# Optimization experiments

Measured on AMD Instinct MI355X. Metric: run time of the kernel, lower is better.

## Reference

```python
import jax, jax.numpy as jnp
import numpy as np

D_MODEL = 1024
N_HEADS = 16
HEAD_DIM = D_MODEL // N_HEADS
THETA = 10000.0


def _rope_tables(seq_len, d_k, dtype):
    pos = jnp.arange(seq_len, dtype=jnp.float32)
    dim = jnp.arange(0, d_k, 2, dtype=jnp.float32)
    inv_freq = 1.0 / (THETA ** (dim / d_k))  # [d_k//2]
    angle = pos[:, None] * inv_freq[None, :]  # [seq, d_k//2]
    return jnp.cos(angle).astype(dtype), jnp.sin(angle).astype(dtype)


def _apply_rope(x, cos, sin):
    # x: [B, H, S, d_k]; cos/sin: [S, d_k//2] (interleaved-pair rotation)
    x1 = x[..., ::2]
    x2 = x[..., 1::2]
    r1 = x1 * cos - x2 * sin
    r2 = x1 * sin + x2 * cos
    out = jnp.stack([r1, r2], axis=-1)  # [..., d_k//2, 2]
    return out.reshape(x.shape)


def setup_inputs() -> dict:
    key = jax.random.key(0)
    ks = jax.random.split(key, 5)
    B, S, D = 4, 2048, D_MODEL
    std = np.sqrt(2.0 / (D + D)).astype(np.float32)
    x = jax.random.normal(ks[0], (B, S, D), dtype=jnp.float32)
    wq = jax.random.normal(ks[1], (D, D), dtype=jnp.float32) * std
    wk = jax.random.normal(ks[2], (D, D), dtype=jnp.float32) * std
    wv = jax.random.normal(ks[3], (D, D), dtype=jnp.float32) * std
    wo = jax.random.normal(ks[4], (D, D), dtype=jnp.float32) * std
    return {"x": x, "wq": wq, "wk": wk, "wv": wv, "wo": wo}


def reference(x, wq, wk, wv, wo):
    B, S, D = x.shape
    H, dk = N_HEADS, HEAD_DIM
    # projections (weight stored [d_out, d_in])
    q = jnp.einsum('oi,bsi->bso', wq, x)
    k = jnp.einsum('oi,bsi->bso', wk, x)
    v = jnp.einsum('oi,bsi->bso', wv, x)
    # split heads -> [B, H, S, dk]
    q = q.reshape(B, S, H, dk).transpose(0, 2, 1, 3)
    k = k.reshape(B, S, H, dk).transpose(0, 2, 1, 3)
    v = v.reshape(B, S, H, dk).transpose(0, 2, 1, 3)
    cos, sin = _rope_tables(S, dk, x.dtype)
    q = _apply_rope(q, cos, sin)
    k = _apply_rope(k, cos, sin)
    scale = 1.0 / np.sqrt(dk)
    logits = jnp.einsum('bhqd,bhkd->bhqk', q, k) * scale
    causal = jnp.tril(jnp.ones((S, S), dtype=bool))
    logits = jnp.where(causal, logits, -jnp.inf)
    probs = jax.nn.softmax(logits, axis=-1)
    ctx = jnp.einsum('bhqk,bhkd->bhqd', probs, v)
    ctx = ctx.transpose(0, 2, 1, 3).reshape(B, S, D)
    return jnp.einsum('oi,bsi->bso', wo, ctx)
```

## Files before the change

### kernel.cpp

```cpp
#include <hip/hip_runtime.h>
#include <hip/hip_bf16.h>
#include <cstdint>
#include <cstddef>


typedef __bf16 bf16;
typedef __bf16 bf16x2 __attribute__((ext_vector_type(2)));
typedef __bf16 bf16x4 __attribute__((ext_vector_type(4)));
typedef __bf16 bf16x8 __attribute__((ext_vector_type(8)));
typedef float  f32x4  __attribute__((ext_vector_type(4)));

#define SEQ 2048
#define NH  16
#define DM  1024
#define MFMA16 __builtin_amdgcn_mfma_f32_16x16x32_bf16

__device__ __forceinline__ void async16(bf16* lds, const bf16* g) {
  __builtin_amdgcn_global_load_lds(
      (__attribute__((address_space(1))) void*)(g),
      (__attribute__((address_space(3))) void*)(lds), 16, 0, 0);
}

__global__ void cvt_all(const float* __restrict__ x,
                        const float* __restrict__ w0, const float* __restrict__ w1,
                        const float* __restrict__ w2, const float* __restrict__ w3,
                        bf16* __restrict__ xb, bf16* __restrict__ wb) {
  int i = blockIdx.x * blockDim.x + threadIdx.x;
  float4 f;
  bf16x4* dst;
  if (i < 2097152) {
    f = ((const float4*)x)[i];
    dst = (bf16x4*)xb + i;
  } else {
    int k = i - 2097152;
    int sel = k >> 18, j = k & 262143;
    const float* src = sel == 0 ? w0 : sel == 1 ? w1 : sel == 2 ? w2 : w3;
    f = ((const float4*)src)[j];
    dst = (bf16x4*)wb + k;
  }
  bf16x4 o;
  o.x = (bf16)f.x; o.y = (bf16)f.y; o.z = (bf16)f.z; o.w = (bf16)f.w;
  *dst = o;
}


__global__ void __launch_bounds__(256)
gemm_out(const bf16* __restrict__ A, const bf16* __restrict__ B,
         float* __restrict__ C, int M, int N, int K) {
  __shared__ bf16 As[3][128 * 32];
  __shared__ bf16 Bs[3][128 * 32];
  const int tid  = threadIdx.x;
  const int lane = tid & 63;
  const int w    = tid >> 6;
  const int l15  = lane & 15, g = lane >> 4;
  const int wr   = w >> 1, wc = w & 1;
  const long bm = (long)blockIdx.x * 128, bn = (long)blockIdx.y * 128;

  f32x4 acc[4][4] = {};

  const int r0 = tid >> 2;
  const int c0 = (tid & 3) << 3;
  const bf16* aB = A + (bm + r0) * K + c0;
  const bf16* bB = B + (bn + r0) * K + c0;

#pragma unroll
  for (int t = 0; t < 2; ++t) {
    const bf16* ap = aB + t * 32;
    const bf16* bp = bB + t * 32;
    async16(&As[t][(size_t)tid * 8],        ap);
    async16(&As[t][2048 + (size_t)tid * 8], ap + (size_t)64 * K);
    async16(&Bs[t][(size_t)tid * 8],        bp);
    async16(&Bs[t][2048 + (size_t)tid * 8], bp + (size_t)64 * K);
  }

  const int nkt = K >> 5;
  int cur = 0;
  for (int kt = 0; kt < nkt; ++kt) {
    if (kt + 1 < nkt) asm volatile("s_waitcnt vmcnt(4)" ::: "memory");
    else              asm volatile("s_waitcnt vmcnt(0)" ::: "memory");
    __builtin_amdgcn_s_barrier();
    asm volatile("" ::: "memory");
    if (kt + 2 < nkt) {
      const int nb = (cur == 0) ? 2 : cur - 1;
      const bf16* ap = aB + (kt + 2) * 32;
      const bf16* bp = bB + (kt + 2) * 32;
      async16(&As[nb][(size_t)tid * 8],        ap);
      async16(&As[nb][2048 + (size_t)tid * 8], ap + (size_t)64 * K);
      async16(&Bs[nb][(size_t)tid * 8],        bp);
      async16(&Bs[nb][2048 + (size_t)tid * 8], bp + (size_t)64 * K);
    }
    bf16x8 af[4], bfr[4];
#pragma unroll
    for (int mf = 0; mf < 4; ++mf)
      af[mf] = *(const bf16x8*)&As[cur][(wr * 64 + mf * 16 + l15) * 32 + g * 8];
#pragma unroll
    for (int nf = 0; nf < 4; ++nf)
      bfr[nf] = *(const bf16x8*)&Bs[cur][(wc * 64 + nf * 16 + l15) * 32 + g * 8];
#pragma unroll
    for (int mf = 0; mf < 4; ++mf)
#pragma unroll
      for (int nf = 0; nf < 4; ++nf)
        acc[mf][nf] = MFMA16(af[mf], bfr[nf], acc[mf][nf], 0, 0, 0);
    cur = (cur == 2) ? 0 : cur + 1;
  }

#pragma unroll
  for (int mf = 0; mf < 4; ++mf)
#pragma unroll
    for (int nf = 0; nf < 4; ++nf)
#pragma unroll
      for (int r = 0; r < 4; ++r) {
        long m = bm + wr * 64 + mf * 16 + g * 4 + r;
        long n = bn + wc * 64 + nf * 16 + l15;
        C[m * N + n] = acc[mf][nf][r];
      }
}

__global__ void __launch_bounds__(256)
gemm_qkv(const bf16* __restrict__ A, const bf16* __restrict__ Wqkv,
         bf16* __restrict__ Qo, bf16* __restrict__ Ko, bf16* __restrict__ Vto,
         int M, int K) {
  __shared__ bf16 As[3][128 * 32];
  __shared__ bf16 Bs[3][128 * 32];
  const int tid  = threadIdx.x;
  const int lane = tid & 63;
  const int w    = tid >> 6;
  const int l15  = lane & 15, g = lane >> 4;
  const int wr   = w >> 1, wc = w & 1;
  const long bm  = (long)blockIdx.x * 128;
  const long bnG = (long)blockIdx.y * 128;
  const int region = blockIdx.y >> 3;
  const long bn  = (long)(blockIdx.y & 7) * 128;

  f32x4 acc[4][4] = {};

  const int r0 = tid >> 2;
  const int c0 = (tid & 3) << 3;
  const bf16* aB = A + (bm + r0) * K + c0;
  const bf16* bB = Wqkv + (bnG + r0) * K + c0;

#pragma unroll
  for (int t = 0; t < 2; ++t) {
    const bf16* ap = aB + t * 32;
    const bf16* bp = bB + t * 32;
    async16(&As[t][(size_t)tid * 8],        ap);
    async16(&As[t][2048 + (size_t)tid * 8], ap + (size_t)64 * K);
    async16(&Bs[t][(size_t)tid * 8],        bp);
    async16(&Bs[t][2048 + (size_t)tid * 8], bp + (size_t)64 * K);
  }

  const int nkt = K >> 5;
  int cur = 0;
  for (int kt = 0; kt < nkt; ++kt) {
    if (kt + 1 < nkt) asm volatile("s_waitcnt vmcnt(4)" ::: "memory");
    else              asm volatile("s_waitcnt vmcnt(0)" ::: "memory");
    __builtin_amdgcn_s_barrier();
    asm volatile("" ::: "memory");
    if (kt + 2 < nkt) {
      const int nb = (cur == 0) ? 2 : cur - 1;
      const bf16* ap = aB + (kt + 2) * 32;
      const bf16* bp = bB + (kt + 2) * 32;
      async16(&As[nb][(size_t)tid * 8],        ap);
      async16(&As[nb][2048 + (size_t)tid * 8], ap + (size_t)64 * K);
      async16(&Bs[nb][(size_t)tid * 8],        bp);
      async16(&Bs[nb][2048 + (size_t)tid * 8], bp + (size_t)64 * K);
    }
    bf16x8 af[4], bfr[4];
#pragma unroll
    for (int mf = 0; mf < 4; ++mf)
      af[mf] = *(const bf16x8*)&As[cur][(wr * 64 + mf * 16 + l15) * 32 + g * 8];
#pragma unroll
    for (int nf = 0; nf < 4; ++nf)
      bfr[nf] = *(const bf16x8*)&Bs[cur][(wc * 64 + nf * 16 + l15) * 32 + g * 8];
#pragma unroll
    for (int mf = 0; mf < 4; ++mf)
#pragma unroll
      for (int nf = 0; nf < 4; ++nf)
        acc[mf][nf] = MFMA16(af[mf], bfr[nf], acc[mf][nf], 0, 0, 0);
    cur = (cur == 2) ? 0 : cur + 1;
  }

  if (region < 2) {
    bf16* C = region ? Ko : Qo;
#pragma unroll
    for (int mf = 0; mf < 4; ++mf)
#pragma unroll
      for (int nf = 0; nf < 4; ++nf)
#pragma unroll
        for (int r = 0; r < 4; ++r) {
          long m = bm + wr * 64 + mf * 16 + g * 4 + r;
          long n = bn + wc * 64 + nf * 16 + l15;
          C[m * DM + n] = (bf16)acc[mf][nf][r];
        }
  } else {
#pragma unroll
    for (int mf = 0; mf < 4; ++mf)
#pragma unroll
      for (int nf = 0; nf < 4; ++nf) {
        long s0 = bm + wr * 64 + mf * 16 + g * 4;
        long b  = s0 >> 11;
        long s  = s0 & 2047;
        long n  = bn + wc * 64 + nf * 16 + l15;
        long h  = n >> 6, d = n & 63;
        bf16x4 v;
#pragma unroll
        for (int r = 0; r < 4; ++r) v[r] = (bf16)acc[mf][nf][r];
        *(bf16x4*)&Vto[(((b * NH + h) * 64 + d) << 11) + s] = v;
      }
  }
}

__global__ void rope_k(bf16* __restrict__ K) {
  int i = blockIdx.x * blockDim.x + threadIdx.x;
  size_t e = (size_t)i * 8;
  const int d0 = (int)(e & 63);
  const int s  = (int)((e >> 10) & 2047);
  bf16x8 v = *(bf16x8*)&K[e];
#pragma unroll
  for (int t = 0; t < 4; ++t) {
    const int j = (d0 >> 1) + t;
    float inv = __expf((float)j * -0.2878231366242558f);
    float ang = (float)s * inv;
    float sn, cn;
    __sincosf(ang, &sn, &cn);
    float k1 = (float)v[2 * t], k2 = (float)v[2 * t + 1];
    v[2 * t]     = (bf16)(k1 * cn - k2 * sn);
    v[2 * t + 1] = (bf16)(k1 * sn + k2 * cn);
  }
  *(bf16x8*)&K[e] = v;
}

__global__ void __launch_bounds__(256, 2)
attn_kernel(const bf16* __restrict__ Q, const bf16* __restrict__ Kg,
            const bf16* __restrict__ Vt, bf16* __restrict__ ctx) {
  __shared__ bf16 Ks[2][64 * 64];
  __shared__ bf16 Vs[2][64 * 64];
  __shared__ bf16 Ps[4 * 2048];
  const int tid  = threadIdx.x;
  const int lane = tid & 63, w = tid >> 6;
  const int l15  = lane & 15, g = lane >> 4;
  const int bid  = (int)blockIdx.x;
  const int qts  = 15 - (bid >> 6);
  const int bh   = bid & 63;
  const int b  = bh >> 4, h = bh & 15;
  const int qw = qts * 128 + w * 32;
  const int ktmax = 2 * qts + 1;

  bf16x8 qf[2][2];
#pragma unroll
  for (int qg = 0; qg < 2; ++qg) {
    const int srq = qw + qg * 16 + l15;
    const bf16* qp = Q + ((size_t)(b * SEQ + srq)) * DM + h * 64 + g * 8;
#pragma unroll
    for (int kk = 0; kk < 2; ++kk) {
      bf16x8 v = *(const bf16x8*)(qp + kk * 32);
#pragma unroll
      for (int t = 0; t < 4; ++t) {
        const int j = kk * 16 + g * 4 + t;
        float inv = __expf((float)j * -0.2878231366242558f);
        float ang = (float)srq * inv;
        float sn, cn;
        __sincosf(ang, &sn, &cn);
        float q1 = (float)v[2 * t], q2 = (float)v[2 * t + 1];
        v[2 * t]     = (bf16)((q1 * cn - q2 * sn) * 0.125f);
        v[2 * t + 1] = (bf16)((q1 * sn + q2 * cn) * 0.125f);
      }
      qf[qg][kk] = v;
    }
  }

  f32x4 o[2][4] = {};
  float l_run[2] = {0.f, 0.f};

  const int srow = tid >> 3, scc = tid & 7;
  const int swc  = 8 * (scc ^ (srow & 7));
  const bf16* kb0 = Kg + ((size_t)(b * SEQ + srow)) * DM + h * 64 + swc;
  const bf16* vb0 = Vt + ((size_t)(bh * 64 + srow)) * SEQ + swc;
  bf16* Pw = &Ps[w * 2048];

  async16(&Ks[0][(size_t)tid * 8],        kb0);
  async16(&Ks[0][2048 + (size_t)tid * 8], kb0 + (size_t)32 * DM);
  async16(&Vs[0][(size_t)tid * 8],        vb0);
  async16(&Vs[0][2048 + (size_t)tid * 8], vb0 + (size_t)32 * SEQ);

  for (int kt = 0; kt <= ktmax; ++kt) {
    const int kv0 = kt * 64;
    const int cur = kt & 1, nxt = cur ^ 1;
    __syncthreads();
    if (kt < ktmax) {
      const bf16* kp = kb0 + (size_t)(kt + 1) * 64 * DM;
      const bf16* vp = vb0 + (size_t)(kt + 1) * 64;
      async16(&Ks[nxt][(size_t)tid * 8],        kp);
      async16(&Ks[nxt][2048 + (size_t)tid * 8], kp + (size_t)32 * DM);
      async16(&Vs[nxt][(size_t)tid * 8],        vp);
      async16(&Vs[nxt][2048 + (size_t)tid * 8], vp + (size_t)32 * SEQ);
    }

    if (kv0 > qw + 31) continue;

    f32x4 sa[2][4] = {};
    __builtin_amdgcn_s_setprio(1);
#pragma unroll
    for (int kk = 0; kk < 2; ++kk)
#pragma unroll
      for (int mf = 0; mf < 4; ++mf) {
        const int row = mf * 16 + l15;
        bf16x8 kf = *(const bf16x8*)&Ks[cur][row * 64 + 8 * ((kk * 4 + g) ^ (row & 7))];
        sa[0][mf] = MFMA16(kf, qf[0][kk], sa[0][mf], 0, 0, 0);
        sa[1][mf] = MFMA16(kf, qf[1][kk], sa[1][mf], 0, 0, 0);
      }
    __builtin_amdgcn_s_setprio(0);

#pragma unroll
    for (int j = 0; j < 2; ++j) {
      const int qg = j;
      float p[16];
#pragma unroll
      for (int mf = 0; mf < 4; ++mf)
#pragma unroll
        for (int r = 0; r < 4; ++r) p[mf * 4 + r] = sa[j][mf][r];
      if (kv0 + 63 > qw + qg * 16) {
        const int qidx = qw + qg * 16 + l15;
#pragma unroll
        for (int mf = 0; mf < 4; ++mf)
#pragma unroll
          for (int r = 0; r < 4; ++r)
            if (kv0 + mf * 16 + g * 4 + r > qidx) p[mf * 4 + r] = -1e30f;
      }
      float ts = 0.f;
#pragma unroll
      for (int i = 0; i < 16; ++i) { p[i] = __expf(p[i] - 8.0f); ts += p[i]; }
      l_run[qg] += ts;
#pragma unroll
      for (int mf = 0; mf < 4; ++mf) {
        bf16x4 pv;
#pragma unroll
        for (int r = 0; r < 4; ++r) pv[r] = (bf16)p[mf * 4 + r];
        const int cc = mf * 2 + (g >> 1);
        *(bf16x4*)&Pw[j * 1024 + l15 * 64 + 8 * (cc ^ (l15 & 7)) + (g & 1) * 4] = pv;
      }
    }

    __builtin_amdgcn_s_setprio(1);
#pragma unroll
    for (int kk = 0; kk < 2; ++kk) {
      const int pc = 8 * ((kk * 4 + g) ^ (l15 & 7));
      bf16x8 pa0 = *(const bf16x8*)&Pw[l15 * 64 + pc];
      bf16x8 pa1 = *(const bf16x8*)&Pw[1024 + l15 * 64 + pc];
#pragma unroll
      for (int nf = 0; nf < 4; ++nf) {
        const int vrow = nf * 16 + l15;
        bf16x8 vf = *(const bf16x8*)&Vs[cur][vrow * 64 + 8 * ((kk * 4 + g) ^ (vrow & 7))];
        o[0][nf] = MFMA16(pa0, vf, o[0][nf], 0, 0, 0);
        o[1][nf] = MFMA16(pa1, vf, o[1][nf], 0, 0, 0);
      }
    }
    __builtin_amdgcn_s_setprio(0);
  }

#pragma unroll
  for (int qg = 0; qg < 2; ++qg) {
    float ts = l_run[qg];
    ts += __shfl_xor(ts, 16);
    ts += __shfl_xor(ts, 32);
    float lr[4];
#pragma unroll
    for (int r = 0; r < 4; ++r) lr[r] = 1.0f / __shfl(ts, g * 4 + r);
#pragma unroll
    for (int nf = 0; nf < 4; ++nf)
#pragma unroll
      for (int r = 0; r < 4; ++r) {
        size_t off = ((size_t)(b * SEQ + qw + qg * 16 + g * 4 + r)) * DM + h * 64 + nf * 16 + l15;
        ctx[off] = (bf16)(o[qg][nf][r] * lr[r]);
      }
  }
}

extern "C" void kernel_launch(void* const* d_in, const int* in_sizes, int n_in,
                              void* d_out, int out_size, void* d_ws, size_t ws_size,
                              hipStream_t stream) {
  const float* x  = (const float*)d_in[0];
  const float* wq = (const float*)d_in[1];
  const float* wk = (const float*)d_in[2];
  const float* wv = (const float*)d_in[3];
  const float* wo = (const float*)d_in[4];
  float* out = (float*)d_out;
  char* ws = (char*)d_ws;

  bf16* xb  = (bf16*)(ws);
  bf16* Qb  = (bf16*)(ws + ((size_t)16 << 20));
  bf16* Kb  = (bf16*)(ws + ((size_t)32 << 20));
  bf16* Vt  = (bf16*)(ws + ((size_t)48 << 20));
  bf16* wqb = (bf16*)(ws + ((size_t)64 << 20));
  bf16* wob = (bf16*)(ws + ((size_t)70 << 20));

  cvt_all<<<12288, 256, 0, stream>>>(x, wq, wk, wv, wo, xb, wqb);

  gemm_qkv<<<dim3(64, 24), 256, 0, stream>>>(xb, wqb, Qb, Kb, Vt, 8192, 1024);

  rope_k<<<4096, 256, 0, stream>>>(Kb);

  attn_kernel<<<1024, 256, 0, stream>>>(Qb, Kb, Vt, xb );

  gemm_out<<<dim3(64, 8), 256, 0, stream>>>(xb, wob, out, 8192, 1024, 1024);
}
```

Baseline: 167.2 us.

## Enlarge GEMM tiles to 128x256 with BK=64, swizzled LDS, 512 threads

Both projection GEMMs move from 128x128 tiles with K-step 32 and 4 waves to 128x256 tiles with K-step 64 and 8 waves. Shared-memory rows are XOR-swizzled to avoid bank conflicts, and the loop is split into two half-phases that interleave staging with MFMA issue under raised wave priority. The aim is more data reuse per loaded tile and fewer barriers per unit of work. The cost is a much larger LDS footprint (about 144 KB per block), which limits occupancy, plus fewer blocks in the grid.

```diff
diff --git a/kernel.cpp b/kernel.cpp
--- a/kernel.cpp
+++ b/kernel.cpp
@@ -44,64 +44,87 @@
 }
 
 
-__global__ void __launch_bounds__(256)
+#define STAGEA(bu, kc) { \
+  const bf16* s_ = Abase + (kc); \
+  async16(&SA[bu][(size_t)tid * 8], s_); \
+  async16(&SA[bu][4096 + (size_t)tid * 8], s_ + (size_t)64 * K); }
+#define STAGEB(bu, h, kc) { \
+  const bf16* s_ = Bbase + (size_t)(h) * 128 * K + (kc); \
+  async16(&SB[bu][h][(size_t)tid * 8], s_); \
+  async16(&SB[bu][h][4096 + (size_t)tid * 8], s_ + (size_t)64 * K); }
+
+__global__ void __launch_bounds__(512)
 gemm_out(const bf16* __restrict__ A, const bf16* __restrict__ B,
          float* __restrict__ C, int M, int N, int K) {
-  __shared__ bf16 As[3][128 * 32];
-  __shared__ bf16 Bs[3][128 * 32];
+  __shared__ bf16 SA[3][128 * 64];
+  __shared__ bf16 SB[3][2][128 * 64];
   const int tid  = threadIdx.x;
   const int lane = tid & 63;
   const int w    = tid >> 6;
   const int l15  = lane & 15, g = lane >> 4;
-  const int wr   = w >> 1, wc = w & 1;
-  const long bm = (long)blockIdx.x * 128, bn = (long)blockIdx.y * 128;
+  const int wr   = w >> 2, wc = w & 3;
+  const long bm = (long)blockIdx.x * 128, bn = (long)blockIdx.y * 256;
 
   f32x4 acc[4][4] = {};
 
-  const int r0 = tid >> 2;
-  const int c0 = (tid & 3) << 3;
-  const bf16* aB = A + (bm + r0) * K + c0;
-  const bf16* bB = B + (bn + r0) * K + c0;
-
-#pragma unroll
-  for (int t = 0; t < 2; ++t) {
-    const bf16* ap = aB + t * 32;
-    const bf16* bp = bB + t * 32;
-    async16(&As[t][(size_t)tid * 8],        ap);
-    async16(&As[t][2048 + (size_t)tid * 8], ap + (size_t)64 * K);
-    async16(&Bs[t][(size_t)tid * 8],        bp);
-    async16(&Bs[t][2048 + (size_t)tid * 8], bp + (size_t)64 * K);
-  }
-
-  const int nkt = K >> 5;
-  int cur = 0;
+  const int rowT = tid >> 3;
+  const int csw  = 8 * ((tid & 7) ^ (rowT & 7));
+  const bf16* Abase = A + (size_t)(bm + rowT) * K + csw;
+  const bf16* Bbase = B + (size_t)(bn + rowT) * K + csw;
+
+  STAGEA(0, 0);  STAGEB(0, 0, 0);  STAGEB(0, 1, 0);
+  STAGEA(1, 64); STAGEB(1, 0, 64); STAGEB(1, 1, 64);
+  asm volatile("s_waitcnt vmcnt(6)" ::: "memory");
+  __builtin_amdgcn_s_barrier();
+
+  const int nkt = K >> 6;
+  int cur = 0, stg = 2;
   for (int kt = 0; kt < nkt; ++kt) {
-    if (kt + 1 < nkt) asm volatile("s_waitcnt vmcnt(4)" ::: "memory");
-    else              asm volatile("s_waitcnt vmcnt(0)" ::: "memory");
-    __builtin_amdgcn_s_barrier();
-    asm volatile("" ::: "memory");
-    if (kt + 2 < nkt) {
-      const int nb = (cur == 0) ? 2 : cur - 1;
-      const bf16* ap = aB + (kt + 2) * 32;
-      const bf16* bp = bB + (kt + 2) * 32;
-      async16(&As[nb][(size_t)tid * 8],        ap);
-      async16(&As[nb][2048 + (size_t)tid * 8], ap + (size_t)64 * K);
-      async16(&Bs[nb][(size_t)tid * 8],        bp);
-      async16(&Bs[nb][2048 + (size_t)tid * 8], bp + (size_t)64 * K);
-    }
-    bf16x8 af[4], bfr[4];
-#pragma unroll
-    for (int mf = 0; mf < 4; ++mf)
-      af[mf] = *(const bf16x8*)&As[cur][(wr * 64 + mf * 16 + l15) * 32 + g * 8];
-#pragma unroll
-    for (int nf = 0; nf < 4; ++nf)
-      bfr[nf] = *(const bf16x8*)&Bs[cur][(wc * 64 + nf * 16 + l15) * 32 + g * 8];
-#pragma unroll
-    for (int mf = 0; mf < 4; ++mf)
-#pragma unroll
-      for (int nf = 0; nf < 4; ++nf)
-        acc[mf][nf] = MFMA16(af[mf], bfr[nf], acc[mf][nf], 0, 0, 0);
+    const long kc2 = (long)(kt + 2) * 64;
+    bf16x8 bq[4][2];
+#pragma unroll
+    for (int p = 0; p < 2; ++p) {
+      bf16x8 af[2][2];
+#pragma unroll
+      for (int m2 = 0; m2 < 2; ++m2) {
+        const int hr = wr * 64 + (p * 2 + m2) * 16 + l15;
+        const int rb = hr * 64, sw = hr & 7;
+        af[m2][0] = *(const bf16x8*)&SA[cur][rb + 8 * (g ^ sw)];
+        af[m2][1] = *(const bf16x8*)&SA[cur][rb + 8 * ((4 + g) ^ sw)];
+      }
+      if (p == 0) {
+#pragma unroll
+        for (int nf = 0; nf < 4; ++nf) {
+          const int hr = (wc & 1) * 64 + nf * 16 + l15;
+          const int rb = hr * 64, sw = hr & 7;
+          bq[nf][0] = *(const bf16x8*)&SB[cur][wc >> 1][rb + 8 * (g ^ sw)];
+          bq[nf][1] = *(const bf16x8*)&SB[cur][wc >> 1][rb + 8 * ((4 + g) ^ sw)];
+        }
+      }
+      if (kt + 2 < nkt) {
+        if (p == 0) { STAGEA(stg, kc2); STAGEB(stg, 0, kc2); }
+        else        { STAGEB(stg, 1, kc2); }
+      }
+      asm volatile("" ::: "memory");
+      __builtin_amdgcn_s_barrier();
+      __builtin_amdgcn_s_setprio(1);
+#pragma unroll
+      for (int m2 = 0; m2 < 2; ++m2)
+#pragma unroll
+        for (int nf = 0; nf < 4; ++nf)
+#pragma unroll
+          for (int ks = 0; ks < 2; ++ks)
+            acc[p * 2 + m2][nf] = MFMA16(af[m2][ks], bq[nf][ks], acc[p * 2 + m2][nf], 0, 0, 0);
+      __builtin_amdgcn_s_setprio(0);
+      if (p == 1 && kt + 1 < nkt) {
+        if (kt + 2 < nkt) asm volatile("s_waitcnt vmcnt(6)" ::: "memory");
+        else              asm volatile("s_waitcnt vmcnt(0)" ::: "memory");
+      }
+      __builtin_amdgcn_s_barrier();
+      asm volatile("" ::: "memory");
+    }
     cur = (cur == 2) ? 0 : cur + 1;
+    stg = (stg == 2) ? 0 : stg + 1;
   }
 
 #pragma unroll
@@ -116,68 +139,82 @@
       }
 }
 
-__global__ void __launch_bounds__(256)
+__global__ void __launch_bounds__(512)
 gemm_qkv(const bf16* __restrict__ A, const bf16* __restrict__ Wqkv,
          bf16* __restrict__ Qo, bf16* __restrict__ Ko, bf16* __restrict__ Vto,
          int M, int K) {
-  __shared__ bf16 As[3][128 * 32];
-  __shared__ bf16 Bs[3][128 * 32];
+  __shared__ bf16 SA[3][128 * 64];
+  __shared__ bf16 SB[3][2][128 * 64];
   const int tid  = threadIdx.x;
   const int lane = tid & 63;
   const int w    = tid >> 6;
   const int l15  = lane & 15, g = lane >> 4;
-  const int wr   = w >> 1, wc = w & 1;
+  const int wr   = w >> 2, wc = w & 3;
   const long bm  = (long)blockIdx.x * 128;
-  const long bnG = (long)blockIdx.y * 128;
-  const int region = blockIdx.y >> 3;
-  const long bn  = (long)(blockIdx.y & 7) * 128;
+  const long bnG = (long)blockIdx.y * 256;
+  const int region = blockIdx.y >> 2;
+  const long bn  = (long)(blockIdx.y & 3) * 256;
 
   f32x4 acc[4][4] = {};
 
-  const int r0 = tid >> 2;
-  const int c0 = (tid & 3) << 3;
-  const bf16* aB = A + (bm + r0) * K + c0;
-  const bf16* bB = Wqkv + (bnG + r0) * K + c0;
-
-#pragma unroll
-  for (int t = 0; t < 2; ++t) {
-    const bf16* ap = aB + t * 32;
-    const bf16* bp = bB + t * 32;
-    async16(&As[t][(size_t)tid * 8],        ap);
-    async16(&As[t][2048 + (size_t)tid * 8], ap + (size_t)64 * K);
-    async16(&Bs[t][(size_t)tid * 8],        bp);
-    async16(&Bs[t][2048 + (size_t)tid * 8], bp + (size_t)64 * K);
-  }
-
-  const int nkt = K >> 5;
-  int cur = 0;
+  const int rowT = tid >> 3;
+  const int csw  = 8 * ((tid & 7) ^ (rowT & 7));
+  const bf16* Abase = A    + (size_t)(bm  + rowT) * K + csw;
+  const bf16* Bbase = Wqkv + (size_t)(bnG + rowT) * K + csw;
+
+  STAGEA(0, 0);  STAGEB(0, 0, 0);  STAGEB(0, 1, 0);
+  STAGEA(1, 64); STAGEB(1, 0, 64); STAGEB(1, 1, 64);
+  asm volatile("s_waitcnt vmcnt(6)" ::: "memory");
+  __builtin_amdgcn_s_barrier();
+
+  const int nkt = K >> 6;
+  int cur = 0, stg = 2;
   for (int kt = 0; kt < nkt; ++kt) {
-    if (kt + 1 < nkt) asm volatile("s_waitcnt vmcnt(4)" ::: "memory");
-    else              asm volatile("s_waitcnt vmcnt(0)" ::: "memory");
-    __builtin_amdgcn_s_barrier();
-    asm volatile("" ::: "memory");
-    if (kt + 2 < nkt) {
-      const int nb = (cur == 0) ? 2 : cur - 1;
-      const bf16* ap = aB + (kt + 2) * 32;
-      const bf16* bp = bB + (kt + 2) * 32;
-      async16(&As[nb][(size_t)tid * 8],        ap);
-      async16(&As[nb][2048 + (size_t)tid * 8], ap + (size_t)64 * K);
-      async16(&Bs[nb][(size_t)tid * 8],        bp);
-      async16(&Bs[nb][2048 + (size_t)tid * 8], bp + (size_t)64 * K);
-    }
-    bf16x8 af[4], bfr[4];
-#pragma unroll
-    for (int mf = 0; mf < 4; ++mf)
-      af[mf] = *(const bf16x8*)&As[cur][(wr * 64 + mf * 16 + l15) * 32 + g * 8];
-#pragma unroll
-    for (int nf = 0; nf < 4; ++nf)
-      bfr[nf] = *(const bf16x8*)&Bs[cur][(wc * 64 + nf * 16 + l15) * 32 + g * 8];
-#pragma unroll
-    for (int mf = 0; mf < 4; ++mf)
-#pragma unroll
-      for (int nf = 0; nf < 4; ++nf)
-        acc[mf][nf] = MFMA16(af[mf], bfr[nf], acc[mf][nf], 0, 0, 0);
+    const long kc2 = (long)(kt + 2) * 64;
+    bf16x8 bq[4][2];
+#pragma unroll
+    for (int p = 0; p < 2; ++p) {
+      bf16x8 af[2][2];
+#pragma unroll
+      for (int m2 = 0; m2 < 2; ++m2) {
+        const int hr = wr * 64 + (p * 2 + m2) * 16 + l15;
+        const int rb = hr * 64, sw = hr & 7;
+        af[m2][0] = *(const bf16x8*)&SA[cur][rb + 8 * (g ^ sw)];
+        af[m2][1] = *(const bf16x8*)&SA[cur][rb + 8 * ((4 + g) ^ sw)];
+      }
+      if (p == 0) {
+#pragma unroll
+        for (int nf = 0; nf < 4; ++nf) {
+          const int hr = (wc & 1) * 64 + nf * 16 + l15;
+          const int rb = hr * 64, sw = hr & 7;
+          bq[nf][0] = *(const bf16x8*)&SB[cur][wc >> 1][rb + 8 * (g ^ sw)];
+          bq[nf][1] = *(const bf16x8*)&SB[cur][wc >> 1][rb + 8 * ((4 + g) ^ sw)];
+        }
+      }
+      if (kt + 2 < nkt) {
+        if (p == 0) { STAGEA(stg, kc2); STAGEB(stg, 0, kc2); }
+        else        { STAGEB(stg, 1, kc2); }
+      }
+      asm volatile("" ::: "memory");
+      __builtin_amdgcn_s_barrier();
+      __builtin_amdgcn_s_setprio(1);
+#pragma unroll
+      for (int m2 = 0; m2 < 2; ++m2)
+#pragma unroll
+        for (int nf = 0; nf < 4; ++nf)
+#pragma unroll
+          for (int ks = 0; ks < 2; ++ks)
+            acc[p * 2 + m2][nf] = MFMA16(af[m2][ks], bq[nf][ks], acc[p * 2 + m2][nf], 0, 0, 0);
+      __builtin_amdgcn_s_setprio(0);
+      if (p == 1 && kt + 1 < nkt) {
+        if (kt + 2 < nkt) asm volatile("s_waitcnt vmcnt(6)" ::: "memory");
+        else              asm volatile("s_waitcnt vmcnt(0)" ::: "memory");
+      }
+      __builtin_amdgcn_s_barrier();
+      asm volatile("" ::: "memory");
+    }
     cur = (cur == 2) ? 0 : cur + 1;
+    stg = (stg == 2) ? 0 : stg + 1;
   }
 
   if (region < 2) {
@@ -396,11 +433,11 @@
 
   cvt_all<<<12288, 256, 0, stream>>>(x, wq, wk, wv, wo, xb, wqb);
 
-  gemm_qkv<<<dim3(64, 24), 256, 0, stream>>>(xb, wqb, Qb, Kb, Vt, 8192, 1024);
+  gemm_qkv<<<dim3(64, 12), 512, 0, stream>>>(xb, wqb, Qb, Kb, Vt, 8192, 1024);
 
   rope_k<<<4096, 256, 0, stream>>>(Kb);
 
   attn_kernel<<<1024, 256, 0, stream>>>(Qb, Kb, Vt, xb );
 
-  gemm_out<<<dim3(64, 8), 256, 0, stream>>>(xb, wob, out, 8192, 1024, 1024);
-}
+  gemm_out<<<dim3(64, 4), 512, 0, stream>>>(xb, wob, out, 8192, 1024, 1024);
+}
```

After: 165.8 us. About the same (-0.9%).
